# Performance work log

Measured on AMD Instinct MI355X. Metric: run time of the kernel, lower is better.

Reference implementation:

```python
import jax, jax.numpy as jnp
import numpy as np

# VQ codebook lookup from PhraseModel.vq():
#   dist = ||z[:, None, :] - codebook[None, :, :]||_2  over last axis
#   k = argmin(dist, axis=-1); out = codebook[k]
# We compute squared distances via the expansion ||z||^2 - 2 z.c + ||c||^2
# to avoid materializing the [B, K, D] broadcast difference; argmin over
# squared distance equals argmin over distance, so the output is identical.

B, K, D = 262144, 128, 510

def setup_inputs() -> dict:
    key = jax.random.key(0)
    kz, kc = jax.random.split(key)
    z = jax.random.normal(kz, (B, D), dtype=jnp.float32)
    codebook = jax.random.normal(kc, (K, D), dtype=jnp.float32)
    return {"z": z, "codebook": codebook}

def reference(z, codebook):
    # squared L2 distances, [B, K]
    z_sq = jnp.sum(z * z, axis=-1, keepdims=True)            # [B, 1]
    c_sq = jnp.sum(codebook * codebook, axis=-1)             # [K]
    cross = jnp.einsum('bd,kd->bk', z, codebook)             # [B, K]
    dist2 = z_sq - 2.0 * cross + c_sq[None, :]
    k = jnp.argmin(dist2, axis=-1)                           # [B]
    return codebook[k]                                       # [B, D] gather
```

## Files before the change

kernel.cpp:

```cpp
#include <hip/hip_runtime.h>

#define NB 262144
#define ZD 510
#define NK 128
#define GAP_THR 0.5f
#define CHW 68
#define CHUNK_USH (NK * CHW)
#define CHUNK_U4  (CHUNK_USH / 8)

typedef _Float16 half8 __attribute__((ext_vector_type(8)));
typedef __attribute__((ext_vector_type(16))) float f32x16;

#define WS_CB16_OFF 512
#define WS_CNT_OFF  139776
#define WS_LIST_OFF 139840

__device__ inline ushort f2h(float v) {
    return (ushort)__builtin_bit_cast(short, (_Float16)v);
}

__global__ void prep_kernel(const float* __restrict__ cb, float* __restrict__ csq,
                            ushort* __restrict__ cb16, int* __restrict__ cnt) {
    const int code = blockIdx.x;
    const int tid  = threadIdx.x;
    if (code == 0 && tid == 0) cnt[0] = 0;
    const float* row = cb + (size_t)code * ZD;

    __shared__ double ws_red[4];
    double s = 0.0;
    for (int j = 0; j < 2; ++j) {
        int d = tid + (j << 8);
        if (d < ZD) { double v = (double)row[d]; s = fma(v, v, s); }
    }
#pragma unroll
    for (int m = 1; m <= 32; m <<= 1) s += __shfl_xor(s, m, 64);
    if ((tid & 63) == 0) ws_red[tid >> 6] = s;
    __syncthreads();
    if (tid == 0) csq[code] = (float)(ws_red[0] + ws_red[1] + ws_red[2] + ws_red[3]);

    for (int s2 = tid; s2 < 8 * CHW; s2 += 256) {
        int ch = s2 / CHW, off = s2 - ch * CHW;
        int d  = (ch << 6) + off;
        float v = (off < 64 && d < ZD) ? row[d] : 0.f;
        cb16[ch * CHUNK_USH + code * CHW + off] = f2h(v);
    }
}

__global__ __launch_bounds__(512, 4) void vq_fused(
    const float* __restrict__ z, const float* __restrict__ cb,
    const uint4* __restrict__ cb16, const float* __restrict__ csq,
    int* __restrict__ cnt, int* __restrict__ list, float* __restrict__ out) {
    __shared__ __align__(16) ushort cbb[2][CHUNK_USH];
    __shared__ int km[256];

    const int tid   = threadIdx.x;
    const int lane  = tid & 63;
    const int wv    = tid >> 6;
    const int cmod  = lane & 31;
    const int hi    = lane >> 5;
    const int brow0 = blockIdx.x << 8;
    const int wrow0 = brow0 + (wv << 5);

    f32x16 acc[4];
#pragma unroll
    for (int cf = 0; cf < 4; ++cf)
#pragma unroll
        for (int e = 0; e < 16; ++e) acc[cf][e] = 0.f;

    const float* zrow = z + (size_t)(wrow0 + cmod) * ZD;

    {
        uint4 cr0[3];
#pragma unroll
        for (int i = 0; i < 2; ++i) cr0[i] = cb16[(i << 9) + tid];
        if (tid < 64) cr0[2] = cb16[1024 + tid];
#pragma unroll
        for (int i = 0; i < 2; ++i) ((uint4*)cbb[0])[(i << 9) + tid] = cr0[i];
        if (tid < 64) ((uint4*)cbb[0])[1024 + tid] = cr0[2];
    }

#pragma unroll
    for (int c = 0; c < 8; ++c) {
        const int cur = c & 1, nxt = cur ^ 1;
        __syncthreads();

        const int cg = c << 6;
        float2 zr[16];
#pragma unroll
        for (int t = 0; t < 4; ++t) {
            const int dbase = cg + (t << 4) + (hi << 3);
            zr[t * 4 + 0] = *(const float2*)(zrow + dbase);
            zr[t * 4 + 1] = *(const float2*)(zrow + dbase + 2);
            zr[t * 4 + 2] = *(const float2*)(zrow + dbase + 4);
            zr[t * 4 + 3] = (dbase + 6 < ZD) ? *(const float2*)(zrow + dbase + 6)
                                             : make_float2(0.f, 0.f);
        }
        uint4 cr[3];
        if (c < 7) {
#pragma unroll
            for (int i = 0; i < 2; ++i) cr[i] = cb16[(c + 1) * CHUNK_U4 + (i << 9) + tid];
            if (tid < 64) cr[2] = cb16[(c + 1) * CHUNK_U4 + 1024 + tid];
        }

        half8 afr[4];
#pragma unroll
        for (int t = 0; t < 4; ++t) {
            afr[t][0] = (_Float16)zr[t * 4 + 0].x;
            afr[t][1] = (_Float16)zr[t * 4 + 0].y;
            afr[t][2] = (_Float16)zr[t * 4 + 1].x;
            afr[t][3] = (_Float16)zr[t * 4 + 1].y;
            afr[t][4] = (_Float16)zr[t * 4 + 2].x;
            afr[t][5] = (_Float16)zr[t * 4 + 2].y;
            afr[t][6] = (_Float16)zr[t * 4 + 3].x;
            afr[t][7] = (_Float16)zr[t * 4 + 3].y;
        }

#pragma unroll
        for (int t = 0; t < 4; ++t) {
#pragma unroll
            for (int cf = 0; cf < 4; ++cf) {
                const int bbase = (cf * 32 + cmod) * CHW + (t << 4) + (hi << 3);
                union { uint2 u2[2]; half8 h; } b;
                b.u2[0] = *(const uint2*)&cbb[cur][bbase];
                b.u2[1] = *(const uint2*)&cbb[cur][bbase + 4];
                acc[cf] = __builtin_amdgcn_mfma_f32_32x32x16_f16(afr[t], b.h, acc[cf], 0, 0, 0);
            }
        }

        if (c < 7) {
#pragma unroll
            for (int i = 0; i < 2; ++i) ((uint4*)cbb[nxt])[(i << 9) + tid] = cr[i];
            if (tid < 64) ((uint4*)cbb[nxt])[1024 + tid] = cr[2];
        }
    }

    float cq[4];
#pragma unroll
    for (int cf = 0; cf < 4; ++cf) cq[cf] = csq[cf * 32 + cmod];

#pragma unroll
    for (int reg = 0; reg < 16; ++reg) {
        float bv = fmaf(-2.f, acc[0][reg], cq[0]);
        int   bk = cmod;
        float m2 = 1e30f;
#pragma unroll
        for (int cf = 1; cf < 4; ++cf) {
            float v = fmaf(-2.f, acc[cf][reg], cq[cf]);
            int  kk = cf * 32 + cmod;
            if (v < bv)      { m2 = bv; bv = v; bk = kk; }
            else if (v < m2) { m2 = v; }
        }
#pragma unroll
        for (int m = 1; m <= 16; m <<= 1) {
            float ov  = __shfl_xor(bv, m, 64);
            int   ok  = __shfl_xor(bk, m, 64);
            float om2 = __shfl_xor(m2, m, 64);
            float nm2 = fminf(fmaxf(bv, ov), fminf(m2, om2));
            bool take = (ov < bv) || (ov == bv && ok < bk);
            bv = take ? ov : bv;
            bk = take ? ok : bk;
            m2 = nm2;
        }
        if (cmod == 0) {
            int rloc = (reg & 3) + ((reg >> 2) << 3) + (hi << 2);
            km[(wv << 5) + rloc] = bk;
            if (m2 - bv < GAP_THR) {
                int idx = atomicAdd(cnt, 1);
                list[idx] = wrow0 + rloc;
            }
        }
    }
    __syncthreads();

    const int half = tid >> 7, h = tid & 127;
    for (int rp = 0; rp < 64; ++rp) {
        int row = (rp << 2) + half;
        int k   = km[row] & 127;
        const float2* src = (const float2*)(cb + (size_t)k * ZD);
        float2*       dst = (float2*)(out + (size_t)(brow0 + row) * ZD);
        dst[h] = src[h];
        if (h < 127) dst[128 + h] = src[128 + h];
    }
}

__global__ __launch_bounds__(256) void repair(
    const float* __restrict__ z, const float* __restrict__ cb,
    const float* __restrict__ csq, const int* __restrict__ cnt,
    const int* __restrict__ list, float* __restrict__ out) {
    __shared__ float zsh[4][512];
    const int tid  = threadIdx.x;
    const int wv   = tid >> 6;
    const int lane = tid & 63;
    const int n    = cnt[0];
    const int gw0  = (blockIdx.x << 2) + wv;

    for (int idx = gw0; idx < n; idx += 2048) {
        const int row = list[idx];
        const float* zr = z + (size_t)row * ZD;
#pragma unroll
        for (int j = 0; j < 8; ++j) {
            int d = (j << 6) + lane;
            zsh[wv][d] = (d < ZD) ? zr[d] : 0.f;
        }
        asm volatile("s_waitcnt lgkmcnt(0)" ::: "memory");

        float bv = 1e30f; int bk = 0;
        for (int c = 0; c < NK; ++c) {
            const float* cr = cb + (size_t)c * ZD;
            float s = 0.f;
#pragma unroll
            for (int j = 0; j < 8; ++j) {
                int d = (j << 6) + lane;
                float cv = (d < ZD) ? cr[d] : 0.f;
                s = fmaf(zsh[wv][d], cv, s);
            }
#pragma unroll
            for (int m = 1; m <= 32; m <<= 1) s += __shfl_xor(s, m, 64);
            float sc = fmaf(-2.f, s, csq[c]);
            if (sc < bv) { bv = sc; bk = c; }
        }
        const float2* src = (const float2*)(cb + (size_t)bk * ZD);
        float2*       dst = (float2*)(out + (size_t)row * ZD);
#pragma unroll
        for (int i = 0; i < 4; ++i) {
            int f2 = (i << 6) + lane;
            if (f2 < 255) dst[f2] = src[f2];
        }
    }
}

extern "C" void kernel_launch(void* const* d_in, const int* in_sizes, int n_in,
                              void* d_out, int out_size, void* d_ws, size_t ws_size,
                              hipStream_t stream) {
    const float* z  = (const float*)d_in[0];
    const float* cb = (const float*)d_in[1];
    float*  out  = (float*)d_out;
    float*  csq  = (float*)d_ws;
    ushort* cb16 = (ushort*)((char*)d_ws + WS_CB16_OFF);
    int*    cnt  = (int*)((char*)d_ws + WS_CNT_OFF);
    int*    list = (int*)((char*)d_ws + WS_LIST_OFF);

    prep_kernel<<<NK, 256, 0, stream>>>(cb, csq, cb16, cnt);
    vq_fused<<<NB / 256, 512, 0, stream>>>(z, cb, (const uint4*)cb16, csq, cnt, list, out);
    repair<<<512, 256, 0, stream>>>(z, cb, csq, cnt, list, out);
}
```

Before: 477.5 us.

## Drop LDS codebook staging; read fp16 codebook fragments directly from global/L2

The fp16 codebook is now stored in a new unpadded chunked layout, and each wave reads its MFMA B fragments straight from global memory instead of staging them through double-buffered shared memory. This removes the per-chunk __syncthreads barriers and the LDS footprint, which may raise occupancy. Blocks shrink to 256 threads covering 128 rows. The trade-off is that every wave re-fetches the 128 KB codebook through the caches, which depends on L1/L2 bandwidth and latency.

```diff
diff --git a/kernel.cpp b/kernel.cpp
--- a/kernel.cpp
+++ b/kernel.cpp
@@ -4,16 +4,13 @@
 #define ZD 510
 #define NK 128
 #define GAP_THR 0.5f
-#define CHW 68
-#define CHUNK_USH (NK * CHW)
-#define CHUNK_U4  (CHUNK_USH / 8)
 
 typedef _Float16 half8 __attribute__((ext_vector_type(8)));
 typedef __attribute__((ext_vector_type(16))) float f32x16;
 
 #define WS_CB16_OFF 512
-#define WS_CNT_OFF  139776
-#define WS_LIST_OFF 139840
+#define WS_CNT_OFF  131584
+#define WS_LIST_OFF 131648
 
 __device__ inline ushort f2h(float v) {
     return (ushort)__builtin_bit_cast(short, (_Float16)v);
@@ -38,27 +35,25 @@
     __syncthreads();
     if (tid == 0) csq[code] = (float)(ws_red[0] + ws_red[1] + ws_red[2] + ws_red[3]);
 
-    for (int s2 = tid; s2 < 8 * CHW; s2 += 256) {
-        int ch = s2 / CHW, off = s2 - ch * CHW;
-        int d  = (ch << 6) + off;
-        float v = (off < 64 && d < ZD) ? row[d] : 0.f;
-        cb16[ch * CHUNK_USH + code * CHW + off] = f2h(v);
-    }
-}
-
-__global__ __launch_bounds__(512, 4) void vq_fused(
+    for (int s2 = tid; s2 < 512; s2 += 256) {
+        int c = s2 >> 6, dl = s2 & 63;
+        float v = (s2 < ZD) ? row[s2] : 0.f;
+        cb16[(c << 13) + (code << 6) + dl] = f2h(v);
+    }
+}
+
+__global__ __launch_bounds__(256, 4) void vq_fused(
     const float* __restrict__ z, const float* __restrict__ cb,
-    const uint4* __restrict__ cb16, const float* __restrict__ csq,
+    const ushort* __restrict__ cb16, const float* __restrict__ csq,
     int* __restrict__ cnt, int* __restrict__ list, float* __restrict__ out) {
-    __shared__ __align__(16) ushort cbb[2][CHUNK_USH];
-    __shared__ int km[256];
+    __shared__ int km[128];
 
     const int tid   = threadIdx.x;
     const int lane  = tid & 63;
     const int wv    = tid >> 6;
     const int cmod  = lane & 31;
     const int hi    = lane >> 5;
-    const int brow0 = blockIdx.x << 8;
+    const int brow0 = blockIdx.x << 7;
     const int wrow0 = brow0 + (wv << 5);
 
     f32x16 acc[4];
@@ -67,70 +62,31 @@
 #pragma unroll
         for (int e = 0; e < 16; ++e) acc[cf][e] = 0.f;
 
-    const float* zrow = z + (size_t)(wrow0 + cmod) * ZD;
-
-    {
-        uint4 cr0[3];
-#pragma unroll
-        for (int i = 0; i < 2; ++i) cr0[i] = cb16[(i << 9) + tid];
-        if (tid < 64) cr0[2] = cb16[1024 + tid];
-#pragma unroll
-        for (int i = 0; i < 2; ++i) ((uint4*)cbb[0])[(i << 9) + tid] = cr0[i];
-        if (tid < 64) ((uint4*)cbb[0])[1024 + tid] = cr0[2];
-    }
+    const float2* zs2 = (const float2*)(z + (size_t)(wrow0 + cmod) * ZD);
 
 #pragma unroll
     for (int c = 0; c < 8; ++c) {
-        const int cur = c & 1, nxt = cur ^ 1;
-        __syncthreads();
-
-        const int cg = c << 6;
+        const int f2base = (c << 5) + (hi << 4);
         float2 zr[16];
 #pragma unroll
-        for (int t = 0; t < 4; ++t) {
-            const int dbase = cg + (t << 4) + (hi << 3);
-            zr[t * 4 + 0] = *(const float2*)(zrow + dbase);
-            zr[t * 4 + 1] = *(const float2*)(zrow + dbase + 2);
-            zr[t * 4 + 2] = *(const float2*)(zrow + dbase + 4);
-            zr[t * 4 + 3] = (dbase + 6 < ZD) ? *(const float2*)(zrow + dbase + 6)
-                                             : make_float2(0.f, 0.f);
-        }
-        uint4 cr[3];
-        if (c < 7) {
-#pragma unroll
-            for (int i = 0; i < 2; ++i) cr[i] = cb16[(c + 1) * CHUNK_U4 + (i << 9) + tid];
-            if (tid < 64) cr[2] = cb16[(c + 1) * CHUNK_U4 + 1024 + tid];
-        }
-
-        half8 afr[4];
-#pragma unroll
-        for (int t = 0; t < 4; ++t) {
-            afr[t][0] = (_Float16)zr[t * 4 + 0].x;
-            afr[t][1] = (_Float16)zr[t * 4 + 0].y;
-            afr[t][2] = (_Float16)zr[t * 4 + 1].x;
-            afr[t][3] = (_Float16)zr[t * 4 + 1].y;
-            afr[t][4] = (_Float16)zr[t * 4 + 2].x;
-            afr[t][5] = (_Float16)zr[t * 4 + 2].y;
-            afr[t][6] = (_Float16)zr[t * 4 + 3].x;
-            afr[t][7] = (_Float16)zr[t * 4 + 3].y;
-        }
-
-#pragma unroll
-        for (int t = 0; t < 4; ++t) {
+        for (int i = 0; i < 16; ++i) {
+            if (c == 7 && hi == 1 && i == 15) zr[i] = make_float2(0.f, 0.f);
+            else                               zr[i] = zs2[f2base + i];
+        }
+
+        const ushort* cbc = cb16 + (c << 13) + (cmod << 6) + (hi << 5);
+#pragma unroll
+        for (int m = 0; m < 4; ++m) {
+            half8 a;
+            a[0] = (_Float16)zr[4 * m + 0].x; a[1] = (_Float16)zr[4 * m + 0].y;
+            a[2] = (_Float16)zr[4 * m + 1].x; a[3] = (_Float16)zr[4 * m + 1].y;
+            a[4] = (_Float16)zr[4 * m + 2].x; a[5] = (_Float16)zr[4 * m + 2].y;
+            a[6] = (_Float16)zr[4 * m + 3].x; a[7] = (_Float16)zr[4 * m + 3].y;
 #pragma unroll
             for (int cf = 0; cf < 4; ++cf) {
-                const int bbase = (cf * 32 + cmod) * CHW + (t << 4) + (hi << 3);
-                union { uint2 u2[2]; half8 h; } b;
-                b.u2[0] = *(const uint2*)&cbb[cur][bbase];
-                b.u2[1] = *(const uint2*)&cbb[cur][bbase + 4];
-                acc[cf] = __builtin_amdgcn_mfma_f32_32x32x16_f16(afr[t], b.h, acc[cf], 0, 0, 0);
+                half8 b = *(const half8*)(cbc + (cf << 11) + (m << 3));
+                acc[cf] = __builtin_amdgcn_mfma_f32_32x32x16_f16(a, b, acc[cf], 0, 0, 0);
             }
-        }
-
-        if (c < 7) {
-#pragma unroll
-            for (int i = 0; i < 2; ++i) ((uint4*)cbb[nxt])[(i << 9) + tid] = cr[i];
-            if (tid < 64) ((uint4*)cbb[nxt])[1024 + tid] = cr[2];
         }
     }
 
@@ -174,7 +130,7 @@
 
     const int half = tid >> 7, h = tid & 127;
     for (int rp = 0; rp < 64; ++rp) {
-        int row = (rp << 2) + half;
+        int row = (rp << 1) + half;
         int k   = km[row] & 127;
         const float2* src = (const float2*)(cb + (size_t)k * ZD);
         float2*       dst = (float2*)(out + (size_t)(brow0 + row) * ZD);
@@ -241,6 +197,6 @@
     int*    list = (int*)((char*)d_ws + WS_LIST_OFF);
 
     prep_kernel<<<NK, 256, 0, stream>>>(cb, csq, cb16, cnt);
-    vq_fused<<<NB / 256, 512, 0, stream>>>(z, cb, (const uint4*)cb16, csq, cnt, list, out);
+    vq_fused<<<NB / 128, 256, 0, stream>>>(z, cb, cb16, csq, cnt, list, out);
     repair<<<512, 256, 0, stream>>>(z, cb, csq, cnt, list, out);
 }
```

After: 730.4 us. +53.0%, slower.
